# Performance work log

Hardware: AMD Instinct MI355X
Metric: run time of the kernel (lower is better)

The kernel has to match this reference:

```python
import jax, jax.numpy as jnp
import numpy as np

N = 4096
D = 2048
NUM_CLASSES = 128
MARGIN = 0.5


def setup_inputs() -> dict:
    key = jax.random.key(0)
    k1, k2, k3 = jax.random.split(key, 3)
    modal1_inputs = jax.random.normal(k1, (N, D), dtype=jnp.float32)
    modal2_inputs = jax.random.normal(k2, (N, D), dtype=jnp.float32)
    targets = jax.random.randint(k3, (N,), 0, NUM_CLASSES, dtype=jnp.int32)
    return {"modal1_inputs": modal1_inputs, "modal2_inputs": modal2_inputs, "targets": targets}


def _segment_mean(x, seg_ids, num_segments):
    sums = jax.ops.segment_sum(x, seg_ids, num_segments=num_segments)
    cnts = jax.ops.segment_sum(jnp.ones((x.shape[0],), x.dtype), seg_ids, num_segments=num_segments)
    return sums / jnp.maximum(cnts, 1.0)[:, None]


def _pairwise_dist(a, b):
    # sqrt of clamped squared Euclidean distance, matching compute_dist
    sq = (jnp.sum(a * a, axis=1)[:, None] + jnp.sum(b * b, axis=1)[None, :]
          - 2.0 * jnp.einsum('nd,md->nm', a, b))
    return jnp.sqrt(jnp.maximum(sq, 1e-12))


def _contrastive(d2, d1, label, margin):
    # mean(label * d2^2 + (1-label) * relu(margin - d1)^2)
    return jnp.mean(label * d2 * d2
                    + (1.0 - label) * jnp.square(jnp.maximum(margin - d1, 0.0)))


def reference(modal1_inputs, modal2_inputs, targets):
    # per-label means (segment mean), gathered back per-sample as in the loop
    meanR = _segment_mean(modal1_inputs, targets, NUM_CLASSES)  # [C, D]
    meanT = _segment_mean(modal2_inputs, targets, NUM_CLASSES)  # [C, D]
    centersR = meanR[targets]                                   # [N, D]
    centersT = meanT[targets]                                   # [N, D]
    centers = 0.5 * (centersR + centersT)                       # [N, D]

    label = (targets[:, None] == targets[None, :]).astype(jnp.float32)  # [N, N]

    dist1 = _pairwise_dist(centersR, centers)  # already sqrt'ed, per original
    dist2 = _pairwise_dist(centersT, centers)
    dd1 = jnp.sqrt(dist1 + 1e-10)              # sqrt of sqrt, per original
    dd2 = jnp.sqrt(dist2 + 1e-10)

    loss1 = _contrastive(dist1, dd1, label, MARGIN)
    loss2 = _contrastive(dist2, dd2, label, MARGIN)
    return loss1 + loss2
```

## Files before the change

kernel.cpp:

```cpp
#include <hip/hip_runtime.h>

#define N_SAMPLES 4096
#define DIM 2048
#define NUM_CLASSES 128
#define MARGIN 0.5f


__global__ __launch_bounds__(256) void mean_kernel(
        const float* __restrict__ x1,
        const float* __restrict__ x2,
        const int* __restrict__ targets,
        int* __restrict__ cnt,
        float* __restrict__ meanR,
        float* __restrict__ meanT,
        float* __restrict__ d_out, int out_size) {
    __shared__ int s_rows[N_SAMPLES];
    __shared__ int s_n;
    const int tid = threadIdx.x;
    const int c = blockIdx.y;
    const float* __restrict__ x = (blockIdx.z == 0) ? x1 : x2;
    float* __restrict__ mean    = (blockIdx.z == 0) ? meanR : meanT;

    if (tid == 0) s_n = 0;
    if (blockIdx.x == 0 && blockIdx.y == 0 && blockIdx.z == 0) {
        for (int i = tid; i < out_size; i += 256) d_out[i] = 0.0f;
    }
    __syncthreads();

    const int4* __restrict__ t4 = (const int4*)targets;
    for (int i = tid; i < N_SAMPLES / 4; i += 256) {
        const int4 v = t4[i];
        const int base = i * 4;
        if (v.x == c) s_rows[atomicAdd(&s_n, 1)] = base;
        if (v.y == c) s_rows[atomicAdd(&s_n, 1)] = base + 1;
        if (v.z == c) s_rows[atomicAdd(&s_n, 1)] = base + 2;
        if (v.w == c) s_rows[atomicAdd(&s_n, 1)] = base + 3;
    }
    __syncthreads();
    const int n = s_n;

    const int col = blockIdx.x * 256 + tid;
    const float4* __restrict__ xs = (const float4*)x;
    float ax = 0.0f, ay = 0.0f, az = 0.0f, aw = 0.0f;

#define LOADG(B, g) do {                                               \
        const int _base = (g) * 8;                                     \
        _Pragma("unroll")                                              \
        for (int u = 0; u < 8; ++u) {                                  \
            const int _r = s_rows[_base + u];                          \
            B[u] = xs[(size_t)_r * (DIM / 4) + col];                   \
        }                                                              \
    } while (0)

#define ACCG(B) do {                                                   \
        _Pragma("unroll")                                              \
        for (int u = 0; u < 8; ++u) {                                  \
            ax += B[u].x; ay += B[u].y; az += B[u].z; aw += B[u].w;    \
        }                                                              \
    } while (0)

    const int nfull = n >> 3;
    const int rem   = n & 7;

    float4 T[8];
    if (rem) {
        const int tbase = nfull * 8;
#pragma unroll
        for (int u = 0; u < 8; ++u) {
            const int idx = tbase + ((u < rem) ? u : 0);
            T[u] = xs[(size_t)s_rows[idx] * (DIM / 4) + col];
        }
    }

    if (nfull > 0) {
        float4 bufA[8], bufB[8];
        LOADG(bufA, 0);
        int g = 1;
        for (; g + 1 < nfull; g += 2) {
            LOADG(bufB, g);
            ACCG(bufA);
            LOADG(bufA, g + 1);
            ACCG(bufB);
        }
        if (g < nfull) {
            LOADG(bufB, g);
            ACCG(bufA);
            ACCG(bufB);
        } else {
            ACCG(bufA);
        }
    }

    if (rem) {
#pragma unroll
        for (int u = 0; u < 8; ++u) {
            const float m = (u < rem) ? 1.0f : 0.0f;
            ax = fmaf(T[u].x, m, ax);
            ay = fmaf(T[u].y, m, ay);
            az = fmaf(T[u].z, m, az);
            aw = fmaf(T[u].w, m, aw);
        }
    }
#undef LOADG
#undef ACCG

    const float inv = 1.0f / (float)((n > 0) ? n : 1);
    float4 m; m.x = ax * inv; m.y = ay * inv; m.z = az * inv; m.w = aw * inv;
    ((float4*)mean)[(size_t)c * (DIM / 4) + col] = m;

    if (blockIdx.x == 0 && blockIdx.z == 0 && tid == 0) cnt[c] = n;
}

__device__ __forceinline__ float wave_sum64(float v) {
#pragma unroll
    for (int m = 32; m >= 1; m >>= 1) v += __shfl_xor(v, m, 64);
    return v;
}

__global__ __launch_bounds__(256) void stat_kernel(
        const float* __restrict__ meanR,
        const float* __restrict__ meanT,
        float* __restrict__ stats) {
    const int c = blockIdx.x;
    const int tid = threadIdx.x;
    const float4* __restrict__ r4 = (const float4*)(meanR + (size_t)c * DIM);
    const float4* __restrict__ t4 = (const float4*)(meanT + (size_t)c * DIM);
    float* __restrict__ cpref = stats + NUM_CLASSES;
    float sd = 0.0f;
    for (int i = tid; i < DIM / 4; i += 256) {
        const float4 r = r4[i], t = t4[i];
        if (i < 8) {
            cpref[(i * 4 + 0) * NUM_CLASSES + c] = 0.5f * (r.x + t.x);
            cpref[(i * 4 + 1) * NUM_CLASSES + c] = 0.5f * (r.y + t.y);
            cpref[(i * 4 + 2) * NUM_CLASSES + c] = 0.5f * (r.z + t.z);
            cpref[(i * 4 + 3) * NUM_CLASSES + c] = 0.5f * (r.w + t.w);
        }
        float dx;
        dx = r.x - t.x; sd = fmaf(dx, dx, sd);
        dx = r.y - t.y; sd = fmaf(dx, dx, sd);
        dx = r.z - t.z; sd = fmaf(dx, dx, sd);
        dx = r.w - t.w; sd = fmaf(dx, dx, sd);
    }
    sd = wave_sum64(sd);
    __shared__ float s[4];
    if ((tid & 63) == 0) s[tid >> 6] = sd;
    __syncthreads();
    if (tid == 0)
        stats[c] = 0.25f * ((s[0] + s[1]) + (s[2] + s[3]));
}

__global__ __launch_bounds__(256) void pair_kernel(
        const float* __restrict__ meanR,
        const float* __restrict__ meanT,
        const float* __restrict__ stats,
        const int* __restrict__ cnt,
        float* __restrict__ d_out) {
    const int idx = blockIdx.x * 256 + threadIdx.x;
    const int a = idx >> 7;
    const int b = idx & 127;
    const float* __restrict__ sqd   = stats;
    const float* __restrict__ cpref = stats + NUM_CLASSES;

    const float invN2 = 1.0f / ((float)N_SAMPLES * (float)N_SAMPLES);
    const float w = (float)cnt[a] * (float)cnt[b] * invN2;

    float total;
    if (a == b) {
        const float t = fmaxf(sqd[a], 1e-12f);
        total = w * (t + t);
    } else {
        const float THR = MARGIN * MARGIN * MARGIN * MARGIN;
        float s1 = 0.0f, s2 = 0.0f;
        const float4* __restrict__ ra4 = (const float4*)(meanR + (size_t)a * DIM);
        const float4* __restrict__ ta4 = (const float4*)(meanT + (size_t)a * DIM);
#pragma unroll
        for (int k4 = 0; k4 < 8; ++k4) {
            const float4 rv = ra4[k4];
            const float4 tv = ta4[k4];
            const float c0 = cpref[(k4 * 4 + 0) * NUM_CLASSES + b];
            const float c1 = cpref[(k4 * 4 + 1) * NUM_CLASSES + b];
            const float c2 = cpref[(k4 * 4 + 2) * NUM_CLASSES + b];
            const float c3 = cpref[(k4 * 4 + 3) * NUM_CLASSES + b];
            float d;
            d = rv.x - c0; s1 = fmaf(d, d, s1);
            d = rv.y - c1; s1 = fmaf(d, d, s1);
            d = rv.z - c2; s1 = fmaf(d, d, s1);
            d = rv.w - c3; s1 = fmaf(d, d, s1);
            d = tv.x - c0; s2 = fmaf(d, d, s2);
            d = tv.y - c1; s2 = fmaf(d, d, s2);
            d = tv.z - c2; s2 = fmaf(d, d, s2);
            d = tv.w - c3; s2 = fmaf(d, d, s2);
        }
        float t1 = 0.0f, t2 = 0.0f;
        if ((s1 < THR) | (s2 < THR)) {
            float sq1 = 0.0f, sq2 = 0.0f;
            const float* __restrict__ ra = meanR + (size_t)a * DIM;
            const float* __restrict__ ta = meanT + (size_t)a * DIM;
            const float* __restrict__ rb = meanR + (size_t)b * DIM;
            const float* __restrict__ tb = meanT + (size_t)b * DIM;
            for (int k = 0; k < DIM; ++k) {
                const float cb = 0.5f * (rb[k] + tb[k]);
                const float e1 = ra[k] - cb;
                const float e2 = ta[k] - cb;
                sq1 = fmaf(e1, e1, sq1);
                sq2 = fmaf(e2, e2, sq2);
            }
            sq1 = fmaxf(sq1, 1e-12f);
            sq2 = fmaxf(sq2, 1e-12f);
            const float dd1 = sqrtf(sqrtf(sq1) + 1e-10f);
            const float dd2 = sqrtf(sqrtf(sq2) + 1e-10f);
            const float r1 = fmaxf(MARGIN - dd1, 0.0f);
            const float r2 = fmaxf(MARGIN - dd2, 0.0f);
            t1 = r1 * r1;
            t2 = r2 * r2;
        }
        total = w * (t1 + t2);
    }

    total = wave_sum64(total);
    __shared__ float sp[4];
    if ((threadIdx.x & 63) == 0) sp[threadIdx.x >> 6] = total;
    __syncthreads();
    if (threadIdx.x == 0)
        atomicAdd(d_out, (sp[0] + sp[1]) + (sp[2] + sp[3]));
}

extern "C" void kernel_launch(void* const* d_in, const int* in_sizes, int n_in,
                              void* d_out, int out_size, void* d_ws, size_t ws_size,
                              hipStream_t stream) {
    const float* modal1 = (const float*)d_in[0];
    const float* modal2 = (const float*)d_in[1];
    const int* targets  = (const int*)d_in[2];
    float* out = (float*)d_out;

    char* ws = (char*)d_ws;
    int*   cnt   = (int*)(ws + 0);
    float* meanR = (float*)(ws + 1024);
    float* meanT = (float*)(ws + 1024 + (size_t)NUM_CLASSES * DIM * 4);
    float* stats = (float*)(ws + 1024 + 2 * (size_t)NUM_CLASSES * DIM * 4);

    dim3 gridB(2, NUM_CLASSES, 2);
    mean_kernel<<<gridB, 256, 0, stream>>>(modal1, modal2, targets, cnt,
                                           meanR, meanT, out, out_size);

    stat_kernel<<<NUM_CLASSES, 256, 0, stream>>>(meanR, meanT, stats);

    pair_kernel<<<(NUM_CLASSES * NUM_CLASSES) / 256, 256, 0, stream>>>(
        meanR, meanT, stats, cnt, out);
}
```

Measured before the change: 101.2 us.

## Fuse per-class stats computation into mean kernel, drop stat kernel launch

Merges the stat kernel into the mean kernel. Each block now runs 512 threads: one half handles modal1 and the other modal2 for the same column slice. The halves exchange their means through shared memory to compute partial squared differences and the centre prefix, and pair_kernel sums the two per-slice partials. This removes one kernel launch and the re-read of meanR/meanT, but halves the grid to 256 blocks and adds extra syncs.

```diff
diff --git a/kernel.cpp b/kernel.cpp
--- a/kernel.cpp
+++ b/kernel.cpp
@@ -6,29 +6,35 @@
 #define MARGIN 0.5f
 
 
-__global__ __launch_bounds__(256) void mean_kernel(
+__global__ __launch_bounds__(512) void mean_kernel(
         const float* __restrict__ x1,
         const float* __restrict__ x2,
         const int* __restrict__ targets,
         int* __restrict__ cnt,
         float* __restrict__ meanR,
         float* __restrict__ meanT,
+        float* __restrict__ stats,
         float* __restrict__ d_out, int out_size) {
     __shared__ int s_rows[N_SAMPLES];
     __shared__ int s_n;
+    __shared__ float4 s_T[256];
+    __shared__ float s_p[4];
     const int tid = threadIdx.x;
+    const int half = tid >> 8;
+    const int lane256 = tid & 255;
     const int c = blockIdx.y;
-    const float* __restrict__ x = (blockIdx.z == 0) ? x1 : x2;
-    float* __restrict__ mean    = (blockIdx.z == 0) ? meanR : meanT;
+    const int bx = blockIdx.x;
+    const float* __restrict__ x = half ? x2 : x1;
+    float* __restrict__ mean    = half ? meanT : meanR;
 
     if (tid == 0) s_n = 0;
-    if (blockIdx.x == 0 && blockIdx.y == 0 && blockIdx.z == 0) {
-        for (int i = tid; i < out_size; i += 256) d_out[i] = 0.0f;
+    if (bx == 0 && c == 0) {
+        for (int i = tid; i < out_size; i += 512) d_out[i] = 0.0f;
     }
     __syncthreads();
 
     const int4* __restrict__ t4 = (const int4*)targets;
-    for (int i = tid; i < N_SAMPLES / 4; i += 256) {
+    for (int i = tid; i < N_SAMPLES / 4; i += 512) {
         const int4 v = t4[i];
         const int base = i * 4;
         if (v.x == c) s_rows[atomicAdd(&s_n, 1)] = base;
@@ -39,7 +45,7 @@
     __syncthreads();
     const int n = s_n;
 
-    const int col = blockIdx.x * 256 + tid;
+    const int col = bx * 256 + lane256;
     const float4* __restrict__ xs = (const float4*)x;
     float ax = 0.0f, ay = 0.0f, az = 0.0f, aw = 0.0f;
 
@@ -108,45 +114,41 @@
     float4 m; m.x = ax * inv; m.y = ay * inv; m.z = az * inv; m.w = aw * inv;
     ((float4*)mean)[(size_t)c * (DIM / 4) + col] = m;
 
-    if (blockIdx.x == 0 && blockIdx.z == 0 && tid == 0) cnt[c] = n;
+    if (half) s_T[lane256] = m;
+    __syncthreads();
+
+    if (!half) {
+        const float4 t = s_T[lane256];
+        float part = 0.0f, d;
+        d = m.x - t.x; part = fmaf(d, d, part);
+        d = m.y - t.y; part = fmaf(d, d, part);
+        d = m.z - t.z; part = fmaf(d, d, part);
+        d = m.w - t.w; part = fmaf(d, d, part);
+#pragma unroll
+        for (int s = 32; s >= 1; s >>= 1) part += __shfl_xor(part, s, 64);
+        if ((tid & 63) == 0) s_p[tid >> 6] = part;
+    }
+    __syncthreads();
+    if (tid == 0) {
+        stats[bx * NUM_CLASSES + c] =
+            0.25f * ((s_p[0] + s_p[1]) + (s_p[2] + s_p[3]));
+        if (bx == 0) cnt[c] = n;
+    }
+
+    if (bx == 0 && tid < 8) {
+        float* __restrict__ cpref = stats + 2 * NUM_CLASSES;
+        const float4 t = s_T[tid];
+        cpref[(4 * tid + 0) * NUM_CLASSES + c] = 0.5f * (m.x + t.x);
+        cpref[(4 * tid + 1) * NUM_CLASSES + c] = 0.5f * (m.y + t.y);
+        cpref[(4 * tid + 2) * NUM_CLASSES + c] = 0.5f * (m.z + t.z);
+        cpref[(4 * tid + 3) * NUM_CLASSES + c] = 0.5f * (m.w + t.w);
+    }
 }
 
 __device__ __forceinline__ float wave_sum64(float v) {
 #pragma unroll
     for (int m = 32; m >= 1; m >>= 1) v += __shfl_xor(v, m, 64);
     return v;
-}
-
-__global__ __launch_bounds__(256) void stat_kernel(
-        const float* __restrict__ meanR,
-        const float* __restrict__ meanT,
-        float* __restrict__ stats) {
-    const int c = blockIdx.x;
-    const int tid = threadIdx.x;
-    const float4* __restrict__ r4 = (const float4*)(meanR + (size_t)c * DIM);
-    const float4* __restrict__ t4 = (const float4*)(meanT + (size_t)c * DIM);
-    float* __restrict__ cpref = stats + NUM_CLASSES;
-    float sd = 0.0f;
-    for (int i = tid; i < DIM / 4; i += 256) {
-        const float4 r = r4[i], t = t4[i];
-        if (i < 8) {
-            cpref[(i * 4 + 0) * NUM_CLASSES + c] = 0.5f * (r.x + t.x);
-            cpref[(i * 4 + 1) * NUM_CLASSES + c] = 0.5f * (r.y + t.y);
-            cpref[(i * 4 + 2) * NUM_CLASSES + c] = 0.5f * (r.z + t.z);
-            cpref[(i * 4 + 3) * NUM_CLASSES + c] = 0.5f * (r.w + t.w);
-        }
-        float dx;
-        dx = r.x - t.x; sd = fmaf(dx, dx, sd);
-        dx = r.y - t.y; sd = fmaf(dx, dx, sd);
-        dx = r.z - t.z; sd = fmaf(dx, dx, sd);
-        dx = r.w - t.w; sd = fmaf(dx, dx, sd);
-    }
-    sd = wave_sum64(sd);
-    __shared__ float s[4];
-    if ((tid & 63) == 0) s[tid >> 6] = sd;
-    __syncthreads();
-    if (tid == 0)
-        stats[c] = 0.25f * ((s[0] + s[1]) + (s[2] + s[3]));
 }
 
 __global__ __launch_bounds__(256) void pair_kernel(
@@ -158,15 +160,16 @@
     const int idx = blockIdx.x * 256 + threadIdx.x;
     const int a = idx >> 7;
     const int b = idx & 127;
-    const float* __restrict__ sqd   = stats;
-    const float* __restrict__ cpref = stats + NUM_CLASSES;
+    const float* __restrict__ sqdp  = stats;
+    const float* __restrict__ cpref = stats + 2 * NUM_CLASSES;
 
     const float invN2 = 1.0f / ((float)N_SAMPLES * (float)N_SAMPLES);
     const float w = (float)cnt[a] * (float)cnt[b] * invN2;
 
     float total;
     if (a == b) {
-        const float t = fmaxf(sqd[a], 1e-12f);
+        const float sq = sqdp[a] + sqdp[NUM_CLASSES + a];
+        const float t = fmaxf(sq, 1e-12f);
         total = w * (t + t);
     } else {
         const float THR = MARGIN * MARGIN * MARGIN * MARGIN;
@@ -239,11 +242,9 @@
     float* meanT = (float*)(ws + 1024 + (size_t)NUM_CLASSES * DIM * 4);
     float* stats = (float*)(ws + 1024 + 2 * (size_t)NUM_CLASSES * DIM * 4);
 
-    dim3 gridB(2, NUM_CLASSES, 2);
-    mean_kernel<<<gridB, 256, 0, stream>>>(modal1, modal2, targets, cnt,
-                                           meanR, meanT, out, out_size);
-
-    stat_kernel<<<NUM_CLASSES, 256, 0, stream>>>(meanR, meanT, stats);
+    dim3 gridB(2, NUM_CLASSES);
+    mean_kernel<<<gridB, 512, 0, stream>>>(modal1, modal2, targets, cnt,
+                                           meanR, meanT, stats, out, out_size);
 
     pair_kernel<<<(NUM_CLASSES * NUM_CLASSES) / 256, 256, 0, stream>>>(
         meanR, meanT, stats, cnt, out);
```

Measured after the change: 97.63 us. 3.5% less time.
